# Optimization experiments

Hardware: AMD Instinct MI355X
Metric: run time of the kernel (lower is better)

## Reference

```python
import jax, jax.numpy as jnp
import numpy as np

B, N, K, D = 2, 4096, 20, 128
PH = 8          # pos_mlp hidden dim
AH = 4 * D      # attn_mlp hidden dim (attn_mlp_hidden_mult=4)


def setup_inputs() -> dict:
    key = jax.random.key(0)
    ks = jax.random.split(key, 12)
    s = 0.02
    f32 = jnp.float32
    return {
        "x": jax.random.normal(ks[0], (B, N, 3), f32),
        "pos": jax.random.normal(ks[1], (B, N, 3), f32),
        # linear1/2/3 (torch Linear: y = x @ W.T + b)
        "W1": jax.random.normal(ks[2], (D, 3), f32) * s,  "b1": jnp.zeros((D,), f32),
        "W2": jax.random.normal(ks[3], (D, D), f32) * s,  "b2": jnp.zeros((D,), f32),
        "W3": jax.random.normal(ks[4], (D, D), f32) * s,  "b3": jnp.zeros((D,), f32),
        # PointTransformerLayer params
        "Wqkv": jax.random.normal(ks[5], (3 * D, D), f32) * s,          # to_qkv, no bias
        "Wp1": jax.random.normal(ks[6], (PH, 3), f32) * s,  "bp1": jnp.zeros((PH,), f32),
        "Wp2": jax.random.normal(ks[7], (D, PH), f32) * s,  "bp2": jnp.zeros((D,), f32),
        "Wa1": jax.random.normal(ks[8], (AH, D), f32) * s,  "ba1": jnp.zeros((AH,), f32),
        "Wa2": jax.random.normal(ks[9], (D, AH), f32) * s,  "ba2": jnp.zeros((D,), f32),
    }


def reference(x, pos, W1, b1, W2, b2, W3, b3, Wqkv,
              Wp1, bp1, Wp2, bp2, Wa1, ba1, Wa2, ba2):
    h = x @ W1.T + b1            # [B,N,D] linear1
    h1 = h @ W2.T + b2           # [B,N,D] linear2

    # --- PointTransformerLayer (lucidrains, KNN vector attention) ---
    qkv = h1 @ Wqkv.T            # [B,N,3D]
    q, k, v = jnp.split(qkv, 3, axis=-1)

    # squared pairwise distances and K nearest neighbors (self included)
    d2 = jnp.sum((pos[:, :, None, :] - pos[:, None, :, :]) ** 2, axis=-1)  # [B,N,N]
    _, idx = jax.lax.top_k(-d2, K)                                          # [B,N,K]

    gather = jax.vmap(lambda arr, ind: arr[ind])  # per-batch gather -> [B,N,K,*]
    kn = gather(k, idx)          # [B,N,K,D]
    vn = gather(v, idx)          # [B,N,K,D]
    pn = gather(pos, idx)        # [B,N,K,3]

    rel = pos[:, :, None, :] - pn                                   # [B,N,K,3]
    pe = jax.nn.relu(rel @ Wp1.T + bp1) @ Wp2.T + bp2               # pos_mlp [B,N,K,D]

    vn = vn + pe
    sim = jax.nn.relu((q[:, :, None, :] - kn + pe) @ Wa1.T + ba1) @ Wa2.T + ba2  # attn_mlp
    attn = jax.nn.softmax(sim, axis=2)                              # softmax over neighbors
    agg = jnp.sum(attn * vn, axis=2)                                # [B,N,D]

    return h + (agg @ W3.T + b3)  # residual: x + linear3(x1)
```

## Files before the change

### kernel.cpp

```cpp
#include <hip/hip_runtime.h>
#include <stdint.h>

#define BB 2
#define NN 4096
#define KNB 20
#define DD 128
#define PHH 8
#define AHH 512
#define BN (BB*NN)

typedef unsigned short ushort_t;
typedef short bf16x8 __attribute__((ext_vector_type(8)));
typedef float f32x4 __attribute__((ext_vector_type(4)));

__device__ __forceinline__ uint32_t umin32(uint32_t a, uint32_t b) { return a < b ? a : b; }
__device__ __forceinline__ uint32_t umax32(uint32_t a, uint32_t b) { return a > b ? a : b; }

__device__ __forceinline__ ushort_t f2bf(float f) {
    uint32_t x = __float_as_uint(f);
    return (ushort_t)((x + 0x7FFFu + ((x >> 16) & 1u)) >> 16);
}
__device__ __forceinline__ float bf2f(ushort_t u) {
    union { float f; uint32_t i; } c; c.i = ((uint32_t)u) << 16; return c.f;
}
__device__ __forceinline__ uint32_t cvt_pk_bf16(float lo, float hi) {
    uint32_t r;
    asm("v_cvt_pk_bf16_f32 %0, %1, %2" : "=v"(r) : "v"(lo), "v"(hi));
    return r;
}
__device__ __forceinline__ bf16x8 load_bfrag(const float* __restrict__ src) {
    float4 x = *(const float4*)src;
    float4 y = *(const float4*)(src + 4);
    union { bf16x8 v; uint32_t u[4]; } r;
    r.u[0] = cvt_pk_bf16(x.x, x.y);
    r.u[1] = cvt_pk_bf16(x.z, x.w);
    r.u[2] = cvt_pk_bf16(y.x, y.y);
    r.u[3] = cvt_pk_bf16(y.z, y.w);
    return r.v;
}

#define SW256(m, byteInRow) ((m)*256 + ((byteInRow) ^ (((m)&7) << 4)))
#define SW128(m, byteInRow) ((m)*128 + ((byteInRow) ^ (((m)&7) << 4)))

__global__ __launch_bounds__(256) void k_mega(
        const float* __restrict__ x, const float* __restrict__ pos,
        const float* __restrict__ W1, const float* __restrict__ b1,
        const float* __restrict__ W2f, const float* __restrict__ b2,
        const float* __restrict__ Wqkvf,
        const float* __restrict__ Wa1, const float* __restrict__ Wa2,
        float* __restrict__ h, ushort_t* __restrict__ qf,
        ushort_t* __restrict__ kf, ushort_t* __restrict__ vf,
        int* __restrict__ idx, ushort_t* __restrict__ wbf) {
    __shared__ __align__(16) char smem[16896];
    int tid = threadIdx.x, w = tid >> 6, lane = tid & 63;
    int bid = blockIdx.x;

    if (bid < BN/4) {
        int p = bid*4 + w;
        int b = p >> 12;
        float qx = pos[p*3+0], qy = pos[p*3+1], qz = pos[p*3+2];
        const float* pb = pos + (size_t)b*NN*3;
        uint32_t bk[KNB];
        #pragma unroll
        for (int i = 0; i < KNB; ++i) bk[i] = 0xFFFFFFFFu;
        for (int i = 0; i < NN/64; ++i) {
            int j = i*64 + lane;
            float dx = qx - pb[j*3+0];
            float dy = qy - pb[j*3+1];
            float dz = qz - pb[j*3+2];
            float d2 = dx*dx + dy*dy + dz*dz;
            uint32_t key = (__float_as_uint(d2) & 0xFFFFF000u) | (uint32_t)j;
            if (key < bk[KNB-1]) {
                uint32_t c = key;
                #pragma unroll
                for (int t = 0; t < KNB; ++t) {
                    uint32_t lo = umin32(c, bk[t]);
                    uint32_t hi = umax32(c, bk[t]);
                    bk[t] = lo; c = hi;
                }
            }
        }
        for (int r = 0; r < KNB; ++r) {
            uint32_t m = bk[0];
            #pragma unroll
            for (int s = 1; s < 64; s <<= 1)
                m = umin32(m, (uint32_t)__shfl_xor((int)m, s, 64));
            if (lane == 0) idx[(size_t)p*KNB + r] = (int)(m & 0xFFFu);
            bool win = (bk[0] == m);
            #pragma unroll
            for (int t = 0; t < KNB-1; ++t) bk[t] = win ? bk[t+1] : bk[t];
            bk[KNB-1] = win ? 0xFFFFFFFFu : bk[KNB-1];
        }
    } else if (bid < BN/4 + BN/32) {
        float* xs = (float*)(smem + 16384);
        int p0 = (bid - BN/4) * 32;
        if (tid < 96) xs[tid] = x[(size_t)p0*3 + tid];
        __syncthreads();

        #pragma unroll
        for (int it = 0; it < 16; ++it) {
            int lin = it*256 + tid;
            int m = lin >> 7, d = lin & 127;
            float hv = b1[d] + xs[m*3+0]*W1[d*3+0] + xs[m*3+1]*W1[d*3+1] + xs[m*3+2]*W1[d*3+2];
            h[(size_t)(p0+m)*DD + d] = hv;
            *(ushort_t*)&smem[SW256(m, d*2)] = f2bf(hv);
        }
        __syncthreads();

        {
            f32x4 acc[2][2];
            #pragma unroll
            for (int mt = 0; mt < 2; ++mt)
                #pragma unroll
                for (int ntl = 0; ntl < 2; ++ntl) acc[mt][ntl] = (f32x4){0,0,0,0};
            #pragma unroll
            for (int ks = 0; ks < 4; ++ks) {
                int k0 = ks*32 + (lane >> 4)*8;
                bf16x8 aF[2];
                #pragma unroll
                for (int mt = 0; mt < 2; ++mt)
                    aF[mt] = *(const bf16x8*)&smem[SW256(mt*16 + (lane & 15), k0*2)];
                #pragma unroll
                for (int ntl = 0; ntl < 2; ++ntl) {
                    int n = (2*w + ntl)*16 + (lane & 15);
                    bf16x8 bF = load_bfrag(W2f + (size_t)n*DD + k0);
                    #pragma unroll
                    for (int mt = 0; mt < 2; ++mt)
                        acc[mt][ntl] = __builtin_amdgcn_mfma_f32_16x16x32_bf16(aF[mt], bF, acc[mt][ntl], 0, 0, 0);
                }
            }
            #pragma unroll
            for (int ntl = 0; ntl < 2; ++ntl) {
                int n = (2*w + ntl)*16 + (lane & 15);
                float bias = b2[n];
                #pragma unroll
                for (int mt = 0; mt < 2; ++mt)
                    #pragma unroll
                    for (int i = 0; i < 4; ++i) {
                        int m = mt*16 + (lane >> 4)*4 + i;
                        *(ushort_t*)&smem[8192 + SW256(m, n*2)] = f2bf(acc[mt][ntl][i] + bias);
                    }
            }
        }
        __syncthreads();

        {
            f32x4 acc[2][6];
            #pragma unroll
            for (int mt = 0; mt < 2; ++mt)
                #pragma unroll
                for (int ntl = 0; ntl < 6; ++ntl) acc[mt][ntl] = (f32x4){0,0,0,0};
            #pragma unroll
            for (int ks = 0; ks < 4; ++ks) {
                int k0 = ks*32 + (lane >> 4)*8;
                bf16x8 aF[2];
                #pragma unroll
                for (int mt = 0; mt < 2; ++mt)
                    aF[mt] = *(const bf16x8*)&smem[8192 + SW256(mt*16 + (lane & 15), k0*2)];
                #pragma unroll
                for (int ntl = 0; ntl < 6; ++ntl) {
                    int n = (w*6 + ntl)*16 + (lane & 15);
                    bf16x8 bF = load_bfrag(Wqkvf + (size_t)n*DD + k0);
                    #pragma unroll
                    for (int mt = 0; mt < 2; ++mt)
                        acc[mt][ntl] = __builtin_amdgcn_mfma_f32_16x16x32_bf16(aF[mt], bF, acc[mt][ntl], 0, 0, 0);
                }
            }
            #pragma unroll
            for (int ntl = 0; ntl < 6; ++ntl) {
                int n = (w*6 + ntl)*16 + (lane & 15);
                int r = n >> 7, d = n & 127;
                ushort_t* dst = (r == 0) ? qf : (r == 1) ? kf : vf;
                #pragma unroll
                for (int mt = 0; mt < 2; ++mt)
                    #pragma unroll
                    for (int i = 0; i < 4; ++i) {
                        int m = mt*16 + (lane >> 4)*4 + i;
                        dst[(size_t)(p0+m)*DD + d] = f2bf(acc[mt][ntl][i]);
                    }
            }
        }
    } else {
        int base = (bid - (BN/4 + BN/32)) * 2048 + tid * 8;
        const float* src = (base < 65536) ? (Wa1 + base) : (Wa2 + (base - 65536));
        union { ushort_t u[8]; uint4 q; } pk;
        #pragma unroll
        for (int i = 0; i < 8; ++i) pk.u[i] = f2bf(src[i]);
        *(uint4*)&wbf[base] = pk.q;
    }
}

#define XL_OFF 0
#define TL_OFF 20480
#define PH_OFF 30720
#define NIDX_OFF 32000

__global__ __launch_bounds__(256, 4) void k_attn(
        const float* __restrict__ pos,
        const ushort_t* __restrict__ qf, const ushort_t* __restrict__ kf,
        const ushort_t* __restrict__ vf, const int* __restrict__ idx,
        const float* __restrict__ Wp1, const float* __restrict__ bp1,
        const float* __restrict__ Wp2, const float* __restrict__ bp2,
        const ushort_t* __restrict__ Wa1bf, const float* __restrict__ ba1,
        const ushort_t* __restrict__ Wa2bf, const float* __restrict__ ba2,
        float* __restrict__ agg) {
    __shared__ __align__(16) char smem[32320];
    int* nidx = (int*)(smem + NIDX_OFF);

    int tid = threadIdx.x, w = tid >> 6, lane = tid & 63;
    int lg = lane >> 4, c16 = lane & 15;
    int bid = blockIdx.x;
    int xcd = bid & 7, sloc = bid >> 3;
    int b = xcd >> 2;
    int p0 = b*NN + ((xcd & 3)*256 + sloc)*4;

    if (tid < 80) nidx[tid] = idx[(size_t)(p0 + tid/20)*KNB + (tid%20)];
    __syncthreads();

    if (tid < 80) {
        int m = tid, g = m / 20;
        int j = nidx[m];
        const float* pq = pos + (size_t)(p0+g)*3;
        const float* pn = pos + (size_t)(b*NN+j)*3;
        float r0 = pq[0]-pn[0], r1 = pq[1]-pn[1], r2 = pq[2]-pn[2];
        union { ushort_t u[8]; uint4 q; } pk;
        #pragma unroll
        for (int jj = 0; jj < PHH; ++jj) {
            float a = bp1[jj] + r0*Wp1[jj*3+0] + r1*Wp1[jj*3+1] + r2*Wp1[jj*3+2];
            pk.u[jj] = f2bf(fmaxf(a, 0.f));
        }
        *(uint4*)&smem[PH_OFF + m*16] = pk.q;
    }
    __syncthreads();

    int dA = w*32 + c16, dB = w*32 + 16 + c16;
    float bp2A = bp2[dA], bp2B = bp2[dB];
    float ba2A = ba2[dA], ba2B = ba2[dB];

    bf16x8 bP0 = {0,0,0,0,0,0,0,0}, bP1 = {0,0,0,0,0,0,0,0};
    if (lg == 0) {
        bP0 = load_bfrag(Wp2 + (size_t)dA*PHH);
        bP1 = load_bfrag(Wp2 + (size_t)dB*PHH);
    }

    float qv[4][2];
    #pragma unroll
    for (int g = 0; g < 4; ++g) {
        qv[g][0] = bf2f(qf[(size_t)(p0+g)*DD + dA]);
        qv[g][1] = bf2f(qf[(size_t)(p0+g)*DD + dB]);
    }

    uint32_t vpe_pk[5][4];

    #pragma unroll
    for (int mt = 0; mt < 5; ++mt) {
        bf16x8 aP = {0,0,0,0,0,0,0,0};
        if (lg == 0) aP = *(const bf16x8*)&smem[PH_OFF + (mt*16 + c16)*16];
        f32x4 accP0 = (f32x4){0,0,0,0}, accP1 = (f32x4){0,0,0,0};
        accP0 = __builtin_amdgcn_mfma_f32_16x16x32_bf16(aP, bP0, accP0, 0, 0, 0);
        accP1 = __builtin_amdgcn_mfma_f32_16x16x32_bf16(aP, bP1, accP1, 0, 0, 0);
        float qsA = (mt==0) ? qv[0][0]
                  : (mt==1) ? (lg>=1 ? qv[1][0] : qv[0][0])
                  : (mt==2) ? (lg>=2 ? qv[2][0] : qv[1][0])
                  : (mt==3) ? (lg==3 ? qv[3][0] : qv[2][0])
                  : qv[3][0];
        float qsB = (mt==0) ? qv[0][1]
                  : (mt==1) ? (lg>=1 ? qv[1][1] : qv[0][1])
                  : (mt==2) ? (lg>=2 ? qv[2][1] : qv[1][1])
                  : (mt==3) ? (lg==3 ? qv[3][1] : qv[2][1])
                  : qv[3][1];
        #pragma unroll
        for (int i = 0; i < 4; ++i) {
            int m = mt*16 + lg*4 + i;
            int j = nidx[m];
            const ushort_t* kr = kf + (size_t)(b*NN+j)*DD;
            const ushort_t* vr = vf + (size_t)(b*NN+j)*DD;
            float peA = accP0[i] + bp2A;
            float peB = accP1[i] + bp2B;
            *(ushort_t*)&smem[XL_OFF + SW256(m, dA*2)] = f2bf(qsA - bf2f(kr[dA]) + peA);
            *(ushort_t*)&smem[XL_OFF + SW256(m, dB*2)] = f2bf(qsB - bf2f(kr[dB]) + peB);
            vpe_pk[mt][i] = cvt_pk_bf16(bf2f(vr[dA]) + peA, bf2f(vr[dB]) + peB);
        }
    }
    __syncthreads();

    f32x4 accS[5][2];
    #pragma unroll
    for (int mt = 0; mt < 5; ++mt)
        #pragma unroll
        for (int ntl = 0; ntl < 2; ++ntl) accS[mt][ntl] = (f32x4){0,0,0,0};

    for (int c = 0; c < 8; ++c) {
        f32x4 accB[5];
        #pragma unroll
        for (int mt = 0; mt < 5; ++mt) accB[mt] = (f32x4){0,0,0,0};
        #pragma unroll
        for (int ks = 0; ks < 4; ++ks) {
            int k0 = ks*32 + lg*8;
            bf16x8 aF[5];
            #pragma unroll
            for (int mt = 0; mt < 5; ++mt)
                aF[mt] = *(const bf16x8*)&smem[XL_OFF + SW256(mt*16 + c16, k0*2)];
            bf16x8 bF = *(const bf16x8*)&Wa1bf[(size_t)(c*64 + w*16 + c16)*DD + k0];
            #pragma unroll
            for (int mt = 0; mt < 5; ++mt)
                accB[mt] = __builtin_amdgcn_mfma_f32_16x16x32_bf16(aF[mt], bF, accB[mt], 0, 0, 0);
        }
        {
            int al = w*16 + c16;
            float bias = ba1[c*64 + al];
            #pragma unroll
            for (int mt = 0; mt < 5; ++mt)
                #pragma unroll
                for (int i = 0; i < 4; ++i) {
                    int m = mt*16 + lg*4 + i;
                    *(ushort_t*)&smem[TL_OFF + SW128(m, al*2)] = f2bf(fmaxf(accB[mt][i] + bias, 0.f));
                }
        }
        __syncthreads();

        #pragma unroll
        for (int ks = 0; ks < 2; ++ks) {
            int k0 = ks*32 + lg*8;
            bf16x8 aF[5];
            #pragma unroll
            for (int mt = 0; mt < 5; ++mt)
                aF[mt] = *(const bf16x8*)&smem[TL_OFF + SW128(mt*16 + c16, k0*2)];
            #pragma unroll
            for (int ntl = 0; ntl < 2; ++ntl) {
                int dd = w*32 + ntl*16 + c16;
                bf16x8 bF = *(const bf16x8*)&Wa2bf[(size_t)dd*AHH + c*64 + k0];
                #pragma unroll
                for (int mt = 0; mt < 5; ++mt)
                    accS[mt][ntl] = __builtin_amdgcn_mfma_f32_16x16x32_bf16(aF[mt], bF, accS[mt][ntl], 0, 0, 0);
            }
        }
        __syncthreads();
    }

    float s_mtA[5], a_mtA[5], s_mtB[5], a_mtB[5];
    #pragma unroll
    for (int mt = 0; mt < 5; ++mt) {
        float sa = 0.f, aa = 0.f, sb = 0.f, ab = 0.f;
        #pragma unroll
        for (int i = 0; i < 4; ++i) {
            float eA = __expf(accS[mt][0][i] + ba2A);
            float eB = __expf(accS[mt][1][i] + ba2B);
            uint32_t pk = vpe_pk[mt][i];
            float vA = bf2f((ushort_t)(pk & 0xFFFFu));
            float vB = bf2f((ushort_t)(pk >> 16));
            sa += eA; aa += eA*vA;
            sb += eB; ab += eB*vB;
        }
        s_mtA[mt] = sa; a_mtA[mt] = aa; s_mtB[mt] = sb; a_mtB[mt] = ab;
    }
    bool eq0 = (lg==0), ge1 = (lg>=1), ge2 = (lg>=2), le1 = (lg<=1), le2 = (lg<=2), eq3 = (lg==3);
    float s0A = s_mtA[0] + (eq0 ? s_mtA[1] : 0.f);
    float s1A = (ge1 ? s_mtA[1] : 0.f) + (le1 ? s_mtA[2] : 0.f);
    float s2A = (ge2 ? s_mtA[2] : 0.f) + (le2 ? s_mtA[3] : 0.f);
    float s3A = (eq3 ? s_mtA[3] : 0.f) + s_mtA[4];
    float a0A = a_mtA[0] + (eq0 ? a_mtA[1] : 0.f);
    float a1A = (ge1 ? a_mtA[1] : 0.f) + (le1 ? a_mtA[2] : 0.f);
    float a2A = (ge2 ? a_mtA[2] : 0.f) + (le2 ? a_mtA[3] : 0.f);
    float a3A = (eq3 ? a_mtA[3] : 0.f) + a_mtA[4];
    float s0B = s_mtB[0] + (eq0 ? s_mtB[1] : 0.f);
    float s1B = (ge1 ? s_mtB[1] : 0.f) + (le1 ? s_mtB[2] : 0.f);
    float s2B = (ge2 ? s_mtB[2] : 0.f) + (le2 ? s_mtB[3] : 0.f);
    float s3B = (eq3 ? s_mtB[3] : 0.f) + s_mtB[4];
    float a0B = a_mtB[0] + (eq0 ? a_mtB[1] : 0.f);
    float a1B = (ge1 ? a_mtB[1] : 0.f) + (le1 ? a_mtB[2] : 0.f);
    float a2B = (ge2 ? a_mtB[2] : 0.f) + (le2 ? a_mtB[3] : 0.f);
    float a3B = (eq3 ? a_mtB[3] : 0.f) + a_mtB[4];

    #define RED2(v) { v += __shfl_xor(v, 16, 64); v += __shfl_xor(v, 32, 64); }
    RED2(s0A) RED2(s1A) RED2(s2A) RED2(s3A)
    RED2(a0A) RED2(a1A) RED2(a2A) RED2(a3A)
    RED2(s0B) RED2(s1B) RED2(s2B) RED2(s3B)
    RED2(a0B) RED2(a1B) RED2(a2B) RED2(a3B)
    #undef RED2

    float myS_A = (lg==0) ? s0A : (lg==1) ? s1A : (lg==2) ? s2A : s3A;
    float myA_A = (lg==0) ? a0A : (lg==1) ? a1A : (lg==2) ? a2A : a3A;
    float myS_B = (lg==0) ? s0B : (lg==1) ? s1B : (lg==2) ? s2B : s3B;
    float myA_B = (lg==0) ? a0B : (lg==1) ? a1B : (lg==2) ? a2B : a3B;
    agg[(size_t)(p0+lg)*DD + dA] = myA_A / myS_A;
    agg[(size_t)(p0+lg)*DD + dB] = myA_B / myS_B;
}

__global__ __launch_bounds__(256) void k_out(
        const float* __restrict__ agg, const float* __restrict__ h,
        const float* __restrict__ W3f, const float* __restrict__ b3,
        float* __restrict__ out) {
    __shared__ __align__(16) char smem[8192];
    int tid = threadIdx.x, w = tid >> 6, lane = tid & 63;
    int p0 = blockIdx.x * 32;

    #pragma unroll
    for (int it = 0; it < 16; ++it) {
        int lin = it*256 + tid;
        int m = lin >> 7, d = lin & 127;
        *(ushort_t*)&smem[SW256(m, d*2)] = f2bf(agg[(size_t)(p0+m)*DD + d]);
    }
    __syncthreads();

    f32x4 acc[2][2];
    #pragma unroll
    for (int mt = 0; mt < 2; ++mt)
        #pragma unroll
        for (int ntl = 0; ntl < 2; ++ntl) acc[mt][ntl] = (f32x4){0,0,0,0};
    #pragma unroll
    for (int ks = 0; ks < 4; ++ks) {
        int k0 = ks*32 + (lane >> 4)*8;
        bf16x8 aF[2];
        #pragma unroll
        for (int mt = 0; mt < 2; ++mt)
            aF[mt] = *(const bf16x8*)&smem[SW256(mt*16 + (lane & 15), k0*2)];
        #pragma unroll
        for (int ntl = 0; ntl < 2; ++ntl) {
            int n = (2*w + ntl)*16 + (lane & 15);
            bf16x8 bF = load_bfrag(W3f + (size_t)n*DD + k0);
            #pragma unroll
            for (int mt = 0; mt < 2; ++mt)
                acc[mt][ntl] = __builtin_amdgcn_mfma_f32_16x16x32_bf16(aF[mt], bF, acc[mt][ntl], 0, 0, 0);
        }
    }
    #pragma unroll
    for (int ntl = 0; ntl < 2; ++ntl) {
        int n = (2*w + ntl)*16 + (lane & 15);
        float bias = b3[n];
        #pragma unroll
        for (int mt = 0; mt < 2; ++mt)
            #pragma unroll
            for (int i = 0; i < 4; ++i) {
                int m = mt*16 + (lane >> 4)*4 + i;
                size_t o = (size_t)(p0+m)*DD + n;
                out[o] = acc[mt][ntl][i] + bias + h[o];
            }
    }
}

extern "C" void kernel_launch(void* const* d_in, const int* in_sizes, int n_in,
                              void* d_out, int out_size, void* d_ws, size_t ws_size,
                              hipStream_t stream) {
    const float* x    = (const float*)d_in[0];
    const float* pos  = (const float*)d_in[1];
    const float* W1   = (const float*)d_in[2];
    const float* b1   = (const float*)d_in[3];
    const float* W2   = (const float*)d_in[4];
    const float* b2   = (const float*)d_in[5];
    const float* W3   = (const float*)d_in[6];
    const float* b3   = (const float*)d_in[7];
    const float* Wqkv = (const float*)d_in[8];
    const float* Wp1  = (const float*)d_in[9];
    const float* bp1  = (const float*)d_in[10];
    const float* Wp2  = (const float*)d_in[11];
    const float* bp2  = (const float*)d_in[12];
    const float* Wa1  = (const float*)d_in[13];
    const float* ba1  = (const float*)d_in[14];
    const float* Wa2  = (const float*)d_in[15];
    const float* ba2  = (const float*)d_in[16];

    float* ws = (float*)d_ws;
    float* h   = ws;
    float* agg = ws + (size_t)BN*DD;
    ushort_t* qf = (ushort_t*)(ws + 2*(size_t)BN*DD);
    ushort_t* kf = qf + (size_t)BN*DD;
    ushort_t* vf = qf + 2*(size_t)BN*DD;
    int* idx = (int*)((char*)d_ws + 14680064);
    ushort_t* wbf = (ushort_t*)((char*)d_ws + 15335424);
    ushort_t* Wa1bf = wbf;
    ushort_t* Wa2bf = wbf + 65536;

    k_mega<<<BN/4 + BN/32 + 64, 256, 0, stream>>>(x, pos, W1, b1, W2, b2, Wqkv,
                                                  Wa1, Wa2, h, qf, kf, vf, idx, wbf);
    k_attn<<<BN/4, 256, 0, stream>>>(pos, qf, kf, vf, idx,
                                     Wp1, bp1, Wp2, bp2, Wa1bf, ba1, Wa2bf, ba2, agg);
    k_out <<<BN/32, 256, 0, stream>>>(agg, h, W3, b3, (float*)d_out);
}
```

Before: 174.7 us.

## Precompute per-point Wa1 projections of q and k to skip per-neighbor first attn-MLP GEMM

Uses linearity of the first attention-MLP layer: Wa1·(q - k + pe) becomes Wa1·q + ba1 computed per point, minus Wa1·k per point, plus (Wa1·Wp2)·relu(pos hidden), with the fused weight precomputed. The attention kernel then gathers 512-wide projected k rows per neighbor instead of running the 128→512 GEMM on every neighbor row. This removes most per-neighbor MFMA work for layer one. In exchange it adds larger gather traffic (512 bf16 per neighbor), extra QW/KW workspace writes, and more GEMM work in the prologue kernel. It also replaces f2bf with the hardware pack convert and reorganises the output column mapping into pairs.

```diff
diff --git a/kernel.cpp b/kernel.cpp
--- a/kernel.cpp
+++ b/kernel.cpp
@@ -16,10 +16,6 @@
 __device__ __forceinline__ uint32_t umin32(uint32_t a, uint32_t b) { return a < b ? a : b; }
 __device__ __forceinline__ uint32_t umax32(uint32_t a, uint32_t b) { return a > b ? a : b; }
 
-__device__ __forceinline__ ushort_t f2bf(float f) {
-    uint32_t x = __float_as_uint(f);
-    return (ushort_t)((x + 0x7FFFu + ((x >> 16) & 1u)) >> 16);
-}
 __device__ __forceinline__ float bf2f(ushort_t u) {
     union { float f; uint32_t i; } c; c.i = ((uint32_t)u) << 16; return c.f;
 }
@@ -27,6 +23,9 @@
     uint32_t r;
     asm("v_cvt_pk_bf16_f32 %0, %1, %2" : "=v"(r) : "v"(lo), "v"(hi));
     return r;
+}
+__device__ __forceinline__ ushort_t f2bf(float f) {
+    return (ushort_t)(cvt_pk_bf16(f, f) & 0xFFFFu);
 }
 __device__ __forceinline__ bf16x8 load_bfrag(const float* __restrict__ src) {
     float4 x = *(const float4*)src;
@@ -40,17 +39,18 @@
 }
 
 #define SW256(m, byteInRow) ((m)*256 + ((byteInRow) ^ (((m)&7) << 4)))
-#define SW128(m, byteInRow) ((m)*128 + ((byteInRow) ^ (((m)&7) << 4)))
 
 __global__ __launch_bounds__(256) void k_mega(
         const float* __restrict__ x, const float* __restrict__ pos,
         const float* __restrict__ W1, const float* __restrict__ b1,
         const float* __restrict__ W2f, const float* __restrict__ b2,
         const float* __restrict__ Wqkvf,
-        const float* __restrict__ Wa1, const float* __restrict__ Wa2,
-        float* __restrict__ h, ushort_t* __restrict__ qf,
-        ushort_t* __restrict__ kf, ushort_t* __restrict__ vf,
-        int* __restrict__ idx, ushort_t* __restrict__ wbf) {
+        const float* __restrict__ Wa1f, const float* __restrict__ ba1,
+        const float* __restrict__ Wa2f, const float* __restrict__ Wp2f,
+        float* __restrict__ h, ushort_t* __restrict__ vf,
+        ushort_t* __restrict__ QWbf, ushort_t* __restrict__ KWbf,
+        int* __restrict__ idx, ushort_t* __restrict__ Wa2bf,
+        ushort_t* __restrict__ Wfusebf) {
     __shared__ __align__(16) char smem[16896];
     int tid = threadIdx.x, w = tid >> 6, lane = tid & 63;
     int bid = blockIdx.x;
@@ -94,6 +94,7 @@
     } else if (bid < BN/4 + BN/32) {
         float* xs = (float*)(smem + 16384);
         int p0 = (bid - BN/4) * 32;
+        int lg = lane >> 4, c16 = lane & 15;
         if (tid < 96) xs[tid] = x[(size_t)p0*3 + tid];
         __syncthreads();
 
@@ -115,14 +116,14 @@
                 for (int ntl = 0; ntl < 2; ++ntl) acc[mt][ntl] = (f32x4){0,0,0,0};
             #pragma unroll
             for (int ks = 0; ks < 4; ++ks) {
-                int k0 = ks*32 + (lane >> 4)*8;
+                int k0 = ks*32 + lg*8;
                 bf16x8 aF[2];
                 #pragma unroll
                 for (int mt = 0; mt < 2; ++mt)
-                    aF[mt] = *(const bf16x8*)&smem[SW256(mt*16 + (lane & 15), k0*2)];
+                    aF[mt] = *(const bf16x8*)&smem[SW256(mt*16 + c16, k0*2)];
                 #pragma unroll
                 for (int ntl = 0; ntl < 2; ++ntl) {
-                    int n = (2*w + ntl)*16 + (lane & 15);
+                    int n = (2*w + ntl)*16 + c16;
                     bf16x8 bF = load_bfrag(W2f + (size_t)n*DD + k0);
                     #pragma unroll
                     for (int mt = 0; mt < 2; ++mt)
@@ -131,80 +132,175 @@
             }
             #pragma unroll
             for (int ntl = 0; ntl < 2; ++ntl) {
-                int n = (2*w + ntl)*16 + (lane & 15);
+                int n = (2*w + ntl)*16 + c16;
                 float bias = b2[n];
                 #pragma unroll
                 for (int mt = 0; mt < 2; ++mt)
                     #pragma unroll
                     for (int i = 0; i < 4; ++i) {
-                        int m = mt*16 + (lane >> 4)*4 + i;
+                        int m = mt*16 + lg*4 + i;
                         *(ushort_t*)&smem[8192 + SW256(m, n*2)] = f2bf(acc[mt][ntl][i] + bias);
                     }
             }
         }
         __syncthreads();
 
+        f32x4 acc[2][6];
+        #pragma unroll
+        for (int mt = 0; mt < 2; ++mt)
+            #pragma unroll
+            for (int ntl = 0; ntl < 6; ++ntl) acc[mt][ntl] = (f32x4){0,0,0,0};
+        #pragma unroll
+        for (int ks = 0; ks < 4; ++ks) {
+            int k0 = ks*32 + lg*8;
+            bf16x8 aF[2];
+            #pragma unroll
+            for (int mt = 0; mt < 2; ++mt)
+                aF[mt] = *(const bf16x8*)&smem[8192 + SW256(mt*16 + c16, k0*2)];
+            #pragma unroll
+            for (int ntl = 0; ntl < 6; ++ntl) {
+                int n = (w*6 + ntl)*16 + c16;
+                bf16x8 bF = load_bfrag(Wqkvf + (size_t)n*DD + k0);
+                #pragma unroll
+                for (int mt = 0; mt < 2; ++mt)
+                    acc[mt][ntl] = __builtin_amdgcn_mfma_f32_16x16x32_bf16(aF[mt], bF, acc[mt][ntl], 0, 0, 0);
+            }
+        }
+        #pragma unroll
+        for (int ntl = 0; ntl < 6; ++ntl) {
+            int n = (w*6 + ntl)*16 + c16;
+            int r = n >> 7, d = n & 127;
+            #pragma unroll
+            for (int mt = 0; mt < 2; ++mt)
+                #pragma unroll
+                for (int i = 0; i < 4; ++i) {
+                    int m = mt*16 + lg*4 + i;
+                    if (r == 0) *(ushort_t*)&smem[SW256(m, d*2)] = f2bf(acc[mt][ntl][i]);
+                    else if (r == 2) vf[(size_t)(p0+m)*DD + d] = f2bf(acc[mt][ntl][i]);
+                }
+        }
+        __syncthreads();
+        #pragma unroll
+        for (int ntl = 0; ntl < 6; ++ntl) {
+            int n = (w*6 + ntl)*16 + c16;
+            int r = n >> 7, d = n & 127;
+            if (r == 1) {
+                #pragma unroll
+                for (int mt = 0; mt < 2; ++mt)
+                    #pragma unroll
+                    for (int i = 0; i < 4; ++i) {
+                        int m = mt*16 + lg*4 + i;
+                        *(ushort_t*)&smem[8192 + SW256(m, d*2)] = f2bf(acc[mt][ntl][i]);
+                    }
+            }
+        }
         {
-            f32x4 acc[2][6];
+            f32x4 accQ[2][8];
             #pragma unroll
             for (int mt = 0; mt < 2; ++mt)
                 #pragma unroll
-                for (int ntl = 0; ntl < 6; ++ntl) acc[mt][ntl] = (f32x4){0,0,0,0};
+                for (int ntl = 0; ntl < 8; ++ntl) accQ[mt][ntl] = (f32x4){0,0,0,0};
             #pragma unroll
             for (int ks = 0; ks < 4; ++ks) {
-                int k0 = ks*32 + (lane >> 4)*8;
+                int k0 = ks*32 + lg*8;
                 bf16x8 aF[2];
                 #pragma unroll
                 for (int mt = 0; mt < 2; ++mt)
-                    aF[mt] = *(const bf16x8*)&smem[8192 + SW256(mt*16 + (lane & 15), k0*2)];
-                #pragma unroll
-                for (int ntl = 0; ntl < 6; ++ntl) {
-                    int n = (w*6 + ntl)*16 + (lane & 15);
-                    bf16x8 bF = load_bfrag(Wqkvf + (size_t)n*DD + k0);
+                    aF[mt] = *(const bf16x8*)&smem[SW256(mt*16 + c16, k0*2)];
+                #pragma unroll
+                for (int ntl = 0; ntl < 8; ++ntl) {
+                    int n = (w*8 + ntl)*16 + c16;
+                    bf16x8 bF = load_bfrag(Wa1f + (size_t)n*DD + k0);
                     #pragma unroll
                     for (int mt = 0; mt < 2; ++mt)
-                        acc[mt][ntl] = __builtin_amdgcn_mfma_f32_16x16x32_bf16(aF[mt], bF, acc[mt][ntl], 0, 0, 0);
+                        accQ[mt][ntl] = __builtin_amdgcn_mfma_f32_16x16x32_bf16(aF[mt], bF, accQ[mt][ntl], 0, 0, 0);
                 }
             }
             #pragma unroll
-            for (int ntl = 0; ntl < 6; ++ntl) {
-                int n = (w*6 + ntl)*16 + (lane & 15);
-                int r = n >> 7, d = n & 127;
-                ushort_t* dst = (r == 0) ? qf : (r == 1) ? kf : vf;
+            for (int ntl = 0; ntl < 8; ++ntl) {
+                int n = (w*8 + ntl)*16 + c16;
+                float bias = ba1[n];
                 #pragma unroll
                 for (int mt = 0; mt < 2; ++mt)
                     #pragma unroll
                     for (int i = 0; i < 4; ++i) {
-                        int m = mt*16 + (lane >> 4)*4 + i;
-                        dst[(size_t)(p0+m)*DD + d] = f2bf(acc[mt][ntl][i]);
+                        int m = mt*16 + lg*4 + i;
+                        QWbf[(size_t)(p0+m)*AHH + n] = f2bf(accQ[mt][ntl][i] + bias);
                     }
             }
         }
+        __syncthreads();
+        {
+            f32x4 accK[2][8];
+            #pragma unroll
+            for (int mt = 0; mt < 2; ++mt)
+                #pragma unroll
+                for (int ntl = 0; ntl < 8; ++ntl) accK[mt][ntl] = (f32x4){0,0,0,0};
+            #pragma unroll
+            for (int ks = 0; ks < 4; ++ks) {
+                int k0 = ks*32 + lg*8;
+                bf16x8 aF[2];
+                #pragma unroll
+                for (int mt = 0; mt < 2; ++mt)
+                    aF[mt] = *(const bf16x8*)&smem[8192 + SW256(mt*16 + c16, k0*2)];
+                #pragma unroll
+                for (int ntl = 0; ntl < 8; ++ntl) {
+                    int n = (w*8 + ntl)*16 + c16;
+                    bf16x8 bF = load_bfrag(Wa1f + (size_t)n*DD + k0);
+                    #pragma unroll
+                    for (int mt = 0; mt < 2; ++mt)
+                        accK[mt][ntl] = __builtin_amdgcn_mfma_f32_16x16x32_bf16(aF[mt], bF, accK[mt][ntl], 0, 0, 0);
+                }
+            }
+            #pragma unroll
+            for (int ntl = 0; ntl < 8; ++ntl) {
+                int n = (w*8 + ntl)*16 + c16;
+                #pragma unroll
+                for (int mt = 0; mt < 2; ++mt)
+                    #pragma unroll
+                    for (int i = 0; i < 4; ++i) {
+                        int m = mt*16 + lg*4 + i;
+                        KWbf[(size_t)(p0+m)*AHH + n] = f2bf(accK[mt][ntl][i]);
+                    }
+            }
+        }
+    } else if (bid < BN/4 + BN/32 + 32) {
+        int base = (bid - (BN/4 + BN/32)) * 2048 + tid * 8;
+        union { ushort_t u[8]; uint4 q; } pk;
+        #pragma unroll
+        for (int i = 0; i < 8; ++i) pk.u[i] = f2bf(Wa2f[base + i]);
+        *(uint4*)&Wa2bf[base] = pk.q;
     } else {
-        int base = (bid - (BN/4 + BN/32)) * 2048 + tid * 8;
-        const float* src = (base < 65536) ? (Wa1 + base) : (Wa2 + (base - 65536));
+        int a = (bid - (BN/4 + BN/32 + 32)) * 256 + tid;
+        float s[PHH];
+        #pragma unroll
+        for (int jj = 0; jj < PHH; ++jj) s[jj] = 0.f;
+        for (int d = 0; d < DD; ++d) {
+            float wv = Wa1f[(size_t)a*DD + d];
+            #pragma unroll
+            for (int jj = 0; jj < PHH; ++jj) s[jj] += wv * Wp2f[d*PHH + jj];
+        }
         union { ushort_t u[8]; uint4 q; } pk;
         #pragma unroll
-        for (int i = 0; i < 8; ++i) pk.u[i] = f2bf(src[i]);
-        *(uint4*)&wbf[base] = pk.q;
-    }
-}
-
-#define XL_OFF 0
-#define TL_OFF 20480
-#define PH_OFF 30720
-#define NIDX_OFF 32000
+        for (int jj = 0; jj < PHH; ++jj) pk.u[jj] = f2bf(s[jj]);
+        *(uint4*)&Wfusebf[a*PHH] = pk.q;
+    }
+}
+
+#define TL_OFF 0
+#define PH_OFF 20480
+#define NIDX_OFF 21760
 
 __global__ __launch_bounds__(256, 4) void k_attn(
         const float* __restrict__ pos,
-        const ushort_t* __restrict__ qf, const ushort_t* __restrict__ kf,
+        const ushort_t* __restrict__ QWbf, const ushort_t* __restrict__ KWbf,
         const ushort_t* __restrict__ vf, const int* __restrict__ idx,
         const float* __restrict__ Wp1, const float* __restrict__ bp1,
         const float* __restrict__ Wp2, const float* __restrict__ bp2,
-        const ushort_t* __restrict__ Wa1bf, const float* __restrict__ ba1,
+        const ushort_t* __restrict__ Wfusebf,
         const ushort_t* __restrict__ Wa2bf, const float* __restrict__ ba2,
         float* __restrict__ agg) {
-    __shared__ __align__(16) char smem[32320];
+    __shared__ __align__(16) char smem[22080];
     int* nidx = (int*)(smem + NIDX_OFF);
 
     int tid = threadIdx.x, w = tid >> 6, lane = tid & 63;
@@ -233,7 +329,7 @@
     }
     __syncthreads();
 
-    int dA = w*32 + c16, dB = w*32 + 16 + c16;
+    int dA = w*32 + 2*c16, dB = dA + 1;
     float bp2A = bp2[dA], bp2B = bp2[dB];
     float ba2A = ba2[dA], ba2B = ba2[dB];
 
@@ -242,16 +338,7 @@
         bP0 = load_bfrag(Wp2 + (size_t)dA*PHH);
         bP1 = load_bfrag(Wp2 + (size_t)dB*PHH);
     }
-
-    float qv[4][2];
-    #pragma unroll
-    for (int g = 0; g < 4; ++g) {
-        qv[g][0] = bf2f(qf[(size_t)(p0+g)*DD + dA]);
-        qv[g][1] = bf2f(qf[(size_t)(p0+g)*DD + dB]);
-    }
-
     uint32_t vpe_pk[5][4];
-
     #pragma unroll
     for (int mt = 0; mt < 5; ++mt) {
         bf16x8 aP = {0,0,0,0,0,0,0,0};
@@ -259,30 +346,17 @@
         f32x4 accP0 = (f32x4){0,0,0,0}, accP1 = (f32x4){0,0,0,0};
         accP0 = __builtin_amdgcn_mfma_f32_16x16x32_bf16(aP, bP0, accP0, 0, 0, 0);
         accP1 = __builtin_amdgcn_mfma_f32_16x16x32_bf16(aP, bP1, accP1, 0, 0, 0);
-        float qsA = (mt==0) ? qv[0][0]
-                  : (mt==1) ? (lg>=1 ? qv[1][0] : qv[0][0])
-                  : (mt==2) ? (lg>=2 ? qv[2][0] : qv[1][0])
-                  : (mt==3) ? (lg==3 ? qv[3][0] : qv[2][0])
-                  : qv[3][0];
-        float qsB = (mt==0) ? qv[0][1]
-                  : (mt==1) ? (lg>=1 ? qv[1][1] : qv[0][1])
-                  : (mt==2) ? (lg>=2 ? qv[2][1] : qv[1][1])
-                  : (mt==3) ? (lg==3 ? qv[3][1] : qv[2][1])
-                  : qv[3][1];
         #pragma unroll
         for (int i = 0; i < 4; ++i) {
             int m = mt*16 + lg*4 + i;
             int j = nidx[m];
-            const ushort_t* kr = kf + (size_t)(b*NN+j)*DD;
-            const ushort_t* vr = vf + (size_t)(b*NN+j)*DD;
+            uint32_t vw = *(const uint32_t*)&vf[(size_t)(b*NN+j)*DD + dA];
             float peA = accP0[i] + bp2A;
             float peB = accP1[i] + bp2B;
-            *(ushort_t*)&smem[XL_OFF + SW256(m, dA*2)] = f2bf(qsA - bf2f(kr[dA]) + peA);
-            *(ushort_t*)&smem[XL_OFF + SW256(m, dB*2)] = f2bf(qsB - bf2f(kr[dB]) + peB);
-            vpe_pk[mt][i] = cvt_pk_bf16(bf2f(vr[dA]) + peA, bf2f(vr[dB]) + peB);
-        }
-    }
-    __syncthreads();
+            vpe_pk[mt][i] = cvt_pk_bf16(bf2f((ushort_t)(vw & 0xFFFFu)) + peA,
+                                        bf2f((ushort_t)(vw >> 16)) + peB);
+        }
+    }
 
     f32x4 accS[5][2];
     #pragma unroll
@@ -290,51 +364,72 @@
         #pragma unroll
         for (int ntl = 0; ntl < 2; ++ntl) accS[mt][ntl] = (f32x4){0,0,0,0};
 
-    for (int c = 0; c < 8; ++c) {
-        f32x4 accB[5];
-        #pragma unroll
-        for (int mt = 0; mt < 5; ++mt) accB[mt] = (f32x4){0,0,0,0};
+    for (int c = 0; c < 4; ++c) {
+        int aQ0 = c*128 + dA;
+        bf16x8 bF0 = {0,0,0,0,0,0,0,0}, bF1 = {0,0,0,0,0,0,0,0};
+        if (lg == 0) {
+            bF0 = *(const bf16x8*)&Wfusebf[(size_t)aQ0*PHH];
+            bF1 = *(const bf16x8*)&Wfusebf[(size_t)(aQ0+1)*PHH];
+        }
+        uint32_t qww[4];
+        #pragma unroll
+        for (int g = 0; g < 4; ++g)
+            qww[g] = *(const uint32_t*)&QWbf[(size_t)(p0+g)*AHH + aQ0];
+        uint32_t kwn[4];
+        #pragma unroll
+        for (int i = 0; i < 4; ++i)
+            kwn[i] = *(const uint32_t*)&KWbf[(size_t)(b*NN + nidx[lg*4 + i])*AHH + aQ0];
+        #pragma unroll
+        for (int mt = 0; mt < 5; ++mt) {
+            uint32_t kwc[4];
+            #pragma unroll
+            for (int i = 0; i < 4; ++i) kwc[i] = kwn[i];
+            if (mt < 4) {
+                #pragma unroll
+                for (int i = 0; i < 4; ++i)
+                    kwn[i] = *(const uint32_t*)&KWbf[(size_t)(b*NN + nidx[(mt+1)*16 + lg*4 + i])*AHH + aQ0];
+            }
+            bf16x8 aP = {0,0,0,0,0,0,0,0};
+            if (lg == 0) aP = *(const bf16x8*)&smem[PH_OFF + (mt*16 + c16)*16];
+            f32x4 accF0 = (f32x4){0,0,0,0}, accF1 = (f32x4){0,0,0,0};
+            accF0 = __builtin_amdgcn_mfma_f32_16x16x32_bf16(aP, bF0, accF0, 0, 0, 0);
+            accF1 = __builtin_amdgcn_mfma_f32_16x16x32_bf16(aP, bF1, accF1, 0, 0, 0);
+            uint32_t qsel = (mt==0) ? qww[0]
+                          : (mt==1) ? (lg>=1 ? qww[1] : qww[0])
+                          : (mt==2) ? (lg>=2 ? qww[2] : qww[1])
+                          : (mt==3) ? (lg==3 ? qww[3] : qww[2])
+                          : qww[3];
+            float qA = bf2f((ushort_t)(qsel & 0xFFFFu));
+            float qB = bf2f((ushort_t)(qsel >> 16));
+            #pragma unroll
+            for (int i = 0; i < 4; ++i) {
+                int m = mt*16 + lg*4 + i;
+                float kA = bf2f((ushort_t)(kwc[i] & 0xFFFFu));
+                float kB = bf2f((ushort_t)(kwc[i] >> 16));
+                float tA = fmaxf(qA - kA + accF0[i], 0.f);
+                float tB = fmaxf(qB - kB + accF1[i], 0.f);
+                *(uint32_t*)&smem[TL_OFF + SW256(m, dA*2)] = cvt_pk_bf16(tA, tB);
+            }
+        }
+        __syncthreads();
+
+        __builtin_amdgcn_s_setprio(1);
         #pragma unroll
         for (int ks = 0; ks < 4; ++ks) {
             int k0 = ks*32 + lg*8;
             bf16x8 aF[5];
             #pragma unroll
             for (int mt = 0; mt < 5; ++mt)
-                aF[mt] = *(const bf16x8*)&smem[XL_OFF + SW256(mt*16 + c16, k0*2)];
-            bf16x8 bF = *(const bf16x8*)&Wa1bf[(size_t)(c*64 + w*16 + c16)*DD + k0];
-            #pragma unroll
-            for (int mt = 0; mt < 5; ++mt)
-                accB[mt] = __builtin_amdgcn_mfma_f32_16x16x32_bf16(aF[mt], bF, accB[mt], 0, 0, 0);
-        }
-        {
-            int al = w*16 + c16;
-            float bias = ba1[c*64 + al];
-            #pragma unroll
-            for (int mt = 0; mt < 5; ++mt)
-                #pragma unroll
-                for (int i = 0; i < 4; ++i) {
-                    int m = mt*16 + lg*4 + i;
-                    *(ushort_t*)&smem[TL_OFF + SW128(m, al*2)] = f2bf(fmaxf(accB[mt][i] + bias, 0.f));
-                }
-        }
-        __syncthreads();
-
-        #pragma unroll
-        for (int ks = 0; ks < 2; ++ks) {
-            int k0 = ks*32 + lg*8;
-            bf16x8 aF[5];
-            #pragma unroll
-            for (int mt = 0; mt < 5; ++mt)
-                aF[mt] = *(const bf16x8*)&smem[TL_OFF + SW128(mt*16 + c16, k0*2)];
-            #pragma unroll
-            for (int ntl = 0; ntl < 2; ++ntl) {
-                int dd = w*32 + ntl*16 + c16;
-                bf16x8 bF = *(const bf16x8*)&Wa2bf[(size_t)dd*AHH + c*64 + k0];
-                #pragma unroll
-                for (int mt = 0; mt < 5; ++mt)
-                    accS[mt][ntl] = __builtin_amdgcn_mfma_f32_16x16x32_bf16(aF[mt], bF, accS[mt][ntl], 0, 0, 0);
-            }
-        }
+                aF[mt] = *(const bf16x8*)&smem[TL_OFF + SW256(mt*16 + c16, k0*2)];
+            bf16x8 bW0 = *(const bf16x8*)&Wa2bf[(size_t)dA*AHH + c*128 + k0];
+            bf16x8 bW1 = *(const bf16x8*)&Wa2bf[(size_t)dB*AHH + c*128 + k0];
+            #pragma unroll
+            for (int mt = 0; mt < 5; ++mt) {
+                accS[mt][0] = __builtin_amdgcn_mfma_f32_16x16x32_bf16(aF[mt], bW0, accS[mt][0], 0, 0, 0);
+                accS[mt][1] = __builtin_amdgcn_mfma_f32_16x16x32_bf16(aF[mt], bW1, accS[mt][1], 0, 0, 0);
+            }
+        }
+        __builtin_amdgcn_s_setprio(0);
         __syncthreads();
     }
 
@@ -383,8 +478,10 @@
     float myA_A = (lg==0) ? a0A : (lg==1) ? a1A : (lg==2) ? a2A : a3A;
     float myS_B = (lg==0) ? s0B : (lg==1) ? s1B : (lg==2) ? s2B : s3B;
     float myA_B = (lg==0) ? a0B : (lg==1) ? a1B : (lg==2) ? a2B : a3B;
-    agg[(size_t)(p0+lg)*DD + dA] = myA_A / myS_A;
-    agg[(size_t)(p0+lg)*DD + dB] = myA_B / myS_B;
+    float2 st;
+    st.x = myA_A / myS_A;
+    st.y = myA_B / myS_B;
+    *(float2*)&agg[(size_t)(p0+lg)*DD + dA] = st;
 }
 
 __global__ __launch_bounds__(256) void k_out(
@@ -460,20 +557,20 @@
     const float* Wa2  = (const float*)d_in[15];
     const float* ba2  = (const float*)d_in[16];
 
-    float* ws = (float*)d_ws;
-    float* h   = ws;
-    float* agg = ws + (size_t)BN*DD;
-    ushort_t* qf = (ushort_t*)(ws + 2*(size_t)BN*DD);
-    ushort_t* kf = qf + (size_t)BN*DD;
-    ushort_t* vf = qf + 2*(size_t)BN*DD;
-    int* idx = (int*)((char*)d_ws + 14680064);
-    ushort_t* wbf = (ushort_t*)((char*)d_ws + 15335424);
-    ushort_t* Wa1bf = wbf;
-    ushort_t* Wa2bf = wbf + 65536;
-
-    k_mega<<<BN/4 + BN/32 + 64, 256, 0, stream>>>(x, pos, W1, b1, W2, b2, Wqkv,
-                                                  Wa1, Wa2, h, qf, kf, vf, idx, wbf);
-    k_attn<<<BN/4, 256, 0, stream>>>(pos, qf, kf, vf, idx,
-                                     Wp1, bp1, Wp2, bp2, Wa1bf, ba1, Wa2bf, ba2, agg);
+    char* W = (char*)d_ws;
+    float*    h       = (float*)(W + 0);
+    float*    agg     = (float*)(W + 4194304);
+    ushort_t* vf      = (ushort_t*)(W + 8388608);
+    ushort_t* QWbf    = (ushort_t*)(W + 10485760);
+    ushort_t* KWbf    = (ushort_t*)(W + 18874368);
+    int*      idx     = (int*)(W + 27262976);
+    ushort_t* Wa2bf   = (ushort_t*)(W + 27918336);
+    ushort_t* Wfusebf = (ushort_t*)(W + 28049408);
+
+    k_mega<<<BN/4 + BN/32 + 32 + 2, 256, 0, stream>>>(
+        x, pos, W1, b1, W2, b2, Wqkv, Wa1, ba1, Wa2, Wp2,
+        h, vf, QWbf, KWbf, idx, Wa2bf, Wfusebf);
+    k_attn<<<BN/4, 256, 0, stream>>>(pos, QWbf, KWbf, vf, idx,
+                                     Wp1, bp1, Wp2, bp2, Wfusebf, Wa2bf, ba2, agg);
     k_out <<<BN/32, 256, 0, stream>>>(agg, h, W3, b3, (float*)d_out);
 }
```

Result: slower. 221.2 us (+26.6%).
